# Kernel tuning notes

Hardware: AMD Instinct MI355X
Metric: run time of the kernel (lower is better)

The kernel has to match this reference:

```python
import jax, jax.numpy as jnp
import numpy as np

N_NODES = 50000
N_DIRECTED = 800000  # symmetrized to 1.6M (src,dst) pairs
IN_FEAT = 256
HEADS = 8
OUT = 64


def setup_inputs() -> dict:
    key = jax.random.key(0)
    k1, k2, k3, k4, k5 = jax.random.split(key, 5)
    r = jax.random.randint(k1, (N_DIRECTED,), 0, N_NODES)
    c = jax.random.randint(k2, (N_DIRECTED,), 0, N_NODES)
    # symmetric adjacency (values = 1), as edge list
    src = jnp.concatenate([r, c])
    dst = jnp.concatenate([c, r])
    x = jax.random.normal(k3, (N_NODES, IN_FEAT), dtype=jnp.float32)
    Ws = jax.random.normal(k4, (HEADS, OUT, IN_FEAT), dtype=jnp.float32) * 0.05
    As = jax.random.normal(k5, (HEADS, 2 * OUT, 1), dtype=jnp.float32) * 0.05
    return {"x": x, "src": src, "dst": dst, "Ws": Ws, "As": As}


def reference(x, src, dst, Ws, As):
    H, O, F = Ws.shape
    N = x.shape[0]
    # t_nodes = inputs @ Ws^T  -> [H, N, O]
    t = jnp.einsum('nf,hof->hno', x, Ws)
    a_l = As[:, :O, 0]   # [H, O]
    a_r = As[:, O:, 0]   # [H, O]
    Al = jnp.einsum('hno,ho->hn', t, a_l)  # [H, N]
    Ar = jnp.einsum('hno,ho->hn', t, a_r)  # [H, N]
    outs = []
    for k in range(H):
        # sparse E[i,j] = Al[i] + Ar[j] on adjacency pattern
        e = Al[k][src] + Ar[k][dst]  # [E]
        # NOTE: original applies tf.sparse.softmax to E directly (its lrelu
        # tensor is computed but never used), so no leaky_relu here.
        m = jax.ops.segment_max(e, src, num_segments=N)
        ex = jnp.exp(e - m[src])
        den = jax.ops.segment_sum(ex, src, num_segments=N)
        alpha = ex / den[src]
        # sparse_dense_matmul(alphas, t_nodes[k])
        h = jax.ops.segment_sum(alpha[:, None] * t[k][dst], src, num_segments=N)
        outs.append(h)
    out = jnp.stack(outs, axis=1)          # [N, H, O]
    out = out.reshape(N, H * O)            # reduction=False -> concat heads
    return jax.nn.elu(out)
```

## Files before the change

kernel.cpp:

```cpp
#include <hip/hip_runtime.h>
#include <hip/hip_bf16.h>

#define NN 50000
#define INF 256
#define NH 8
#define OUTF 64
#define NC 512
#define NTILES 782
#define EPB 8192
#define NBK 391
#define NBX 12501

typedef __attribute__((ext_vector_type(8))) short bf16x8;
typedef __attribute__((ext_vector_type(4))) float f32x4;
typedef __attribute__((ext_vector_type(2))) float v2f;
typedef __attribute__((ext_vector_type(8))) float f32x8;

__device__ __forceinline__ unsigned short f2bf(float f){
  unsigned u = __float_as_uint(f);
  u += 0x7FFFu + ((u>>16)&1u);
  return (unsigned short)(u>>16);
}

#define GLOAD_LDS16(g, s) \
  __builtin_amdgcn_global_load_lds((const __attribute__((address_space(1))) void*)(g), \
                                   (__attribute__((address_space(3))) void*)(s), 16, 0, 0)

__global__ void k_atil(const float* __restrict__ W, const float* __restrict__ As,
                       float* __restrict__ atil, int* __restrict__ cursor){
  const int h = blockIdx.x, f = threadIdx.x;
  if (h==0 && f==0){ cursor[0]=0; cursor[1]=0; }
  float s = 0.f;
  for (int o=0;o<64;o++) s += W[((long)h*64+o)*INF + f] * As[h*128 + 64 + o];
  atil[h*256 + f] = s;
}

__global__ __launch_bounds__(256) void k_front(const float* __restrict__ x,
                                               const float* __restrict__ W,
                                               unsigned short* __restrict__ Wt,
                                               const float* __restrict__ atil,
                                               unsigned short* __restrict__ xb,
                                               float* __restrict__ eAr,
                                               const int* __restrict__ src,
                                               int* __restrict__ M,
                                               int E, int NB){
  __shared__ int hh[NBK];
  const int tid = threadIdx.x;
  const int bid = blockIdx.x;
  if (bid < 8){
    const int r = tid>>2, cb = (tid&3)*64;
    char* tile = (char*)(Wt + (size_t)bid*16384);
    const float* Wr = W + ((long)bid*64 + r)*INF;
#pragma unroll
    for (int i=0;i<16;i++){
      int c = cb + i*4;
      float4 v = *(const float4*)(Wr + c);
      ushort4 b; b.x=f2bf(v.x); b.y=f2bf(v.y); b.z=f2bf(v.z); b.w=f2bf(v.w);
      int addr = r*512 + ((((c>>3) ^ (r&7)))<<4) + ((c&7)<<1);
      *(ushort4*)(tile + addr) = b;
    }
    return;
  }
  if (bid < 8+NB){
    const int b = bid-8;
    for (int i=tid;i<NBK;i+=256) hh[i]=0;
    __syncthreads();
    const int base = b*EPB;
    const int lim = min(E-base, EPB);
    for (int i=tid;i<lim;i+=256) atomicAdd(&hh[src[base+i]>>7], 1);
    __syncthreads();
    for (int i=tid;i<NBK;i+=256) M[(long)i*NB + b] = hh[i];
    return;
  }
  const int w = tid>>6, l = tid&63;
  const long n = (long)(bid-8-NB)*4 + w;
  if (n > NN) return;
  if (n == NN){
    uint2 z; z.x=0; z.y=0;
    *(uint2*)((char*)xb + (size_t)n*512 + l*8) = z;
    if (l < 8) eAr[n*NH + l] = 0.f;
    return;
  }
  float4 v = *(const float4*)(x + n*INF + l*4);
  uint2 d;
  d.x = (unsigned)f2bf(v.x) | ((unsigned)f2bf(v.y)<<16);
  d.y = (unsigned)f2bf(v.z) | ((unsigned)f2bf(v.w)<<16);
  *(uint2*)((char*)xb + (size_t)n*512 + l*8) = d;
  float p[8];
#pragma unroll
  for (int h=0;h<8;h++){
    float4 a = *(const float4*)(atil + h*256 + l*4);
    p[h] = v.x*a.x + v.y*a.y + v.z*a.z + v.w*a.w;
  }
#pragma unroll
  for (int off=1; off<64; off<<=1){
#pragma unroll
    for (int h=0;h<8;h++) p[h] += __shfl_xor(p[h], off, 64);
  }
  if (l < 8){
    float e = p[0];
#pragma unroll
    for (int h=1;h<8;h++) if (l==h) e = p[h];
    eAr[n*NH + l] = __expf(e);
  }
}

__global__ __launch_bounds__(256) void k_bscan(int* __restrict__ M,
                                               int* __restrict__ bOff,
                                               int* __restrict__ bEnd,
                                               int* __restrict__ cursor, int NB){
  __shared__ int lds[256];
  __shared__ int sb;
  const int k = blockIdx.x, tid = threadIdx.x;
  int v = (tid<NB) ? M[(long)k*NB+tid] : 0;
  const int orig = v;
  lds[tid]=v; __syncthreads();
  for (int off=1; off<256; off<<=1){
    int a = (tid>=off)? lds[tid-off] : 0;
    __syncthreads(); lds[tid]+=a; __syncthreads();
  }
  if (tid==255){
    int tot = lds[255];
    int base = atomicAdd(&cursor[0], tot);
    sb = base;
    bOff[k] = base;
    bEnd[k] = base + tot;
  }
  __syncthreads();
  if (tid<NB) M[(long)k*NB+tid] = sb + lds[tid]-orig;
}

__global__ __launch_bounds__(256) void k_bscat(const int* __restrict__ src,
                                               const int* __restrict__ dst,
                                               const int* __restrict__ M,
                                               unsigned* __restrict__ ebuf,
                                               int E, int NB){
  __shared__ int cur[NBK];
  const int tid = threadIdx.x, b = blockIdx.x;
  for (int i=tid;i<NBK;i+=256) cur[i] = M[(long)i*NB + b];
  __syncthreads();
  const int base = b*EPB;
  const int lim = min(E-base, EPB);
  for (int i=tid;i<lim;i+=256){
    int s = src[base+i], d = dst[base+i];
    int p = atomicAdd(&cur[s>>7], 1);
    ebuf[p] = ((unsigned)d<<7) | (unsigned)(s&127);
  }
}

__global__ __launch_bounds__(256) void k_bcnt_final(const unsigned* __restrict__ ebuf,
                                                    const int* __restrict__ bOff,
                                                    const int* __restrict__ bEnd,
                                                    int* __restrict__ rbeg,
                                                    int* __restrict__ rend,
                                                    int* __restrict__ col,
                                                    int* __restrict__ cursor){
  __shared__ int h[128];
  __shared__ int s[128];
  __shared__ int cur[128];
  __shared__ int pend[128];
  __shared__ int sb;
  const int k = blockIdx.x, tid = threadIdx.x;
  if (tid<128) h[tid]=0;
  __syncthreads();
  const int beg = bOff[k], end = bEnd[k];
  for (int i=beg+tid; i<end; i+=256)
    atomicAdd(&h[(int)(ebuf[i] & 127u)], 1);
  __syncthreads();
  int pc = 0;
  if (tid<128){
    pc = (h[tid]+7)&~7;
    s[tid] = pc;
  }
  __syncthreads();
  for (int off=1; off<128; off<<=1){
    int a = (tid>=off && tid<128)? s[tid-off] : 0;
    __syncthreads();
    if (tid<128) s[tid] += a;
    __syncthreads();
  }
  if (tid==0){
    sb = atomicAdd(&cursor[1], s[127]);
  }
  __syncthreads();
  if (tid<128){
    int rp = sb + s[tid] - pc;
    rbeg[(k<<7)+tid] = rp;
    rend[(k<<7)+tid] = rp + pc;
    cur[tid] = rp;
    pend[tid] = rp + pc;
  }
  __syncthreads();
  for (int i=beg+tid; i<end; i+=256){
    unsigned e = ebuf[i];
    int p = atomicAdd(&cur[e & 127u], 1);
    col[p] = (int)(e>>7);
  }
  __syncthreads();
  if (tid<128){
    for (int i=cur[tid]; i<pend[tid]; i++) col[i] = NN;
  }
}

__global__ __launch_bounds__(256) void k_aggr2(const int* __restrict__ rbeg,
                                               const int* __restrict__ rend,
                                               const int* __restrict__ col,
                                               const unsigned short* __restrict__ xb,
                                               const float* __restrict__ eAr,
                                               unsigned short* __restrict__ g,
                                               float* __restrict__ den,
                                               int tile0){
  const int tid = threadIdx.x, l = tid&63;
  const int wv = tid>>6;
  const int fh = wv&1;
  const long n = (long)tile0*64 + blockIdx.x*2 + (wv>>1);
  if (n >= NN) return;
  const int beg = __builtin_amdgcn_readfirstlane(rbeg[n]);
  const int end = __builtin_amdgcn_readfirstlane(rend[n]);
  const char* xbp = (const char*)xb + fh*256;
  v2f acc[8] = {};
  float dnl = 0.f;
  const long l4 = (long)l*4;
  const int lw = l&7;

  for (int i=beg; i<end; i+=8){
    int cc[8];
#pragma unroll
    for (int e=0;e<8;e++) cc[e] = __builtin_amdgcn_readfirstlane(col[i+e]);
    unsigned q[8];
#pragma unroll
    for (int e=0;e<8;e++) q[e] = *(const unsigned*)(xbp + (size_t)cc[e]*512 + l4);
    float wl[8];
#pragma unroll
    for (int e=0;e<8;e++) wl[e] = eAr[(size_t)cc[e]*NH + lw];
#pragma unroll
    for (int e=0;e<8;e++) dnl += wl[e];
#pragma unroll
    for (int e=0;e<8;e++){
      f32x8 wv8 = *(const f32x8*)(eAr + (size_t)cc[e]*NH);
      v2f f01;
      f01.x = __uint_as_float(q[e]<<16);
      f01.y = __uint_as_float(q[e]&0xffff0000u);
#pragma unroll
      for (int h=0;h<8;h++){
        v2f w2; w2.x = wv8[h]; w2.y = wv8[h];
        acc[h] = __builtin_elementwise_fma(w2, f01, acc[h]);
      }
    }
  }

  const int lt = (int)(n>>6) - tile0;
  const int r  = (int)(n&63);
  char* tb = (char*)g + (size_t)lt*262144 + r*512 + fh*256 + l*4;
#pragma unroll
  for (int h=0;h<8;h++){
    unsigned d = (unsigned)f2bf(acc[h].x) | ((unsigned)f2bf(acc[h].y)<<16);
    *(unsigned*)(tb + h*32768) = d;
  }
  if (fh==0 && l < 8) den[n*NH + l] = dnl;
}

__global__ __launch_bounds__(256) void k_gemm2(const unsigned short* __restrict__ g,
                                               const unsigned short* __restrict__ Wt,
                                               const float* __restrict__ den,
                                               float* __restrict__ out,
                                               int tile0){
  __shared__ unsigned short As[16384];
  __shared__ unsigned short Bs[16384];
  __shared__ float linv[64];
  const int tid = threadIdx.x, w = tid>>6, l = tid&63;
  const int brow = tile0 + blockIdx.x;
  const int h = blockIdx.y;
  {
    const char* gb = (const char*)g + (size_t)blockIdx.x*262144 + h*32768;
    char* dstA = (char*)As + w*8192;
#pragma unroll
    for (int k=0;k<8;k++){
      int r = w*16 + k*2 + (l>>5);
      const char* sA = gb + r*512 + (((l&31) ^ (r&7))<<4);
      GLOAD_LDS16(sA, dstA + k*1024);
    }
    const char* srcB = (const char*)Wt + (size_t)h*32768 + w*8192 + l*16;
    char* dstB = (char*)Bs + w*8192;
#pragma unroll
    for (int k=0;k<8;k++) GLOAD_LDS16(srcB + k*1024, dstB + k*1024);
  }
  if (tid < 64){
    long gr = (long)brow*64 + tid;
    float dv = (gr < NN) ? den[gr*NH + h] : 1.f;
    linv[tid] = dv > 0.f ? 1.f/dv : 0.f;
  }
  asm volatile("s_waitcnt vmcnt(0)");
  __syncthreads();

  const int col = w*16 + (l&15);
  f32x4 acc[4] = {};
#pragma unroll
  for (int ks=0; ks<8; ks++){
    int chunkB = (ks*4 + (l>>4)) ^ (col&7);
    bf16x8 bfrag = *(const bf16x8*)((char*)Bs + col*512 + (chunkB<<4));
#pragma unroll
    for (int mt=0; mt<4; mt++){
      int ar_ = mt*16 + (l&15);
      int chunkA = (ks*4 + (l>>4)) ^ (ar_&7);
      bf16x8 afrag = *(const bf16x8*)((char*)As + ar_*512 + (chunkA<<4));
      acc[mt] = __builtin_amdgcn_mfma_f32_16x16x32_bf16(afrag, bfrag, acc[mt], 0,0,0);
    }
  }
#pragma unroll
  for (int mt=0; mt<4; mt++){
#pragma unroll
    for (int j=0;j<4;j++){
      int r = mt*16 + (l>>4)*4 + j;
      long gr = (long)brow*64 + r;
      if (gr < NN){
        float v = acc[mt][j] * linv[r];
        out[gr*NC + h*64 + col] = v>0.f ? v : expm1f(v);
      }
    }
  }
}

extern "C" void kernel_launch(void* const* d_in, const int* in_sizes, int n_in,
                              void* d_out, int out_size, void* d_ws, size_t ws_size,
                              hipStream_t stream){
  const float* x   = (const float*)d_in[0];
  const int*   src = (const int*)d_in[1];
  const int*   dst = (const int*)d_in[2];
  const float* Ws  = (const float*)d_in[3];
  const float* Av  = (const float*)d_in[4];
  const int E = in_sizes[1];
  const int NB = (E + EPB - 1) / EPB;

  char* ws = (char*)d_ws;
  size_t off = 0;
  auto alloc = [&](size_t bytes)->void*{
    void* p = ws + off; off += (bytes + 255) & ~(size_t)255; return p;
  };
  unsigned short* xb   = (unsigned short*)alloc((size_t)50048*512);
  float* eAr           = (float*)alloc((size_t)50048*NH*4);
  float* atil          = (float*)alloc(8*256*4);
  float* den           = (float*)alloc((size_t)50048*NH*4);
  unsigned short* Wt   = (unsigned short*)alloc((size_t)8*32768);
  int*   rbeg          = (int*)alloc(50304*4);
  int*   rend          = (int*)alloc(50304*4);
  int*   M             = (int*)alloc((size_t)NBK*256*4);
  int*   bOff          = (int*)alloc(512*4);
  int*   bEnd          = (int*)alloc(512*4);
  int*   cursor        = (int*)alloc(256);
  int*   col           = (int*)alloc(((size_t)E + 8*50048 + 64)*4);

  size_t remain = (ws_size > off + 256) ? (ws_size - off - 256) : 0;
  int chunk = (int)(remain / 262144);
  if (chunk > NTILES) chunk = NTILES;
  if (chunk < 25) chunk = 25;
  unsigned short* g = (unsigned short*)alloc((size_t)chunk*262144);
  unsigned* ebuf = (unsigned*)g;

  k_atil<<<8,256,0,stream>>>(Ws, Av, atil, cursor);
  k_front<<<8+NB+NBX,256,0,stream>>>(x, Ws, Wt, atil, xb, eAr, src, M, E, NB);
  k_bscan<<<NBK,256,0,stream>>>(M, bOff, bEnd, cursor, NB);
  k_bscat<<<NB,256,0,stream>>>(src, dst, M, ebuf, E, NB);
  k_bcnt_final<<<NBK,256,0,stream>>>(ebuf, bOff, bEnd, rbeg, rend, col, cursor);

  int tile0 = 0;
  while (tile0 < NTILES){
    int tiles = NTILES - tile0 < chunk ? NTILES - tile0 : chunk;
    k_aggr2<<<tiles*32,256,0,stream>>>(rbeg, rend, col, xb, eAr, g, den, tile0);
    k_gemm2<<<dim3(tiles,8),256,0,stream>>>(g, Wt, den, (float*)d_out, tile0);
    tile0 += tiles;
  }
}
```

Baseline: 312.3 us.

## Fuse neighbor aggregation and per-head GEMM into one kernel via LDS staging

```diff
diff --git a/kernel.cpp b/kernel.cpp
--- a/kernel.cpp
+++ b/kernel.cpp
@@ -6,7 +6,7 @@
 #define NH 8
 #define OUTF 64
 #define NC 512
-#define NTILES 782
+#define NGB 3128
 #define EPB 8192
 #define NBK 391
 #define NBX 12501
@@ -21,10 +21,6 @@
   u += 0x7FFFu + ((u>>16)&1u);
   return (unsigned short)(u>>16);
 }
-
-#define GLOAD_LDS16(g, s) \
-  __builtin_amdgcn_global_load_lds((const __attribute__((address_space(1))) void*)(g), \
-                                   (__attribute__((address_space(3))) void*)(s), 16, 0, 0)
 
 __global__ void k_atil(const float* __restrict__ W, const float* __restrict__ As,
                        float* __restrict__ atil, int* __restrict__ cursor){
@@ -202,120 +198,93 @@
   }
 }
 
-__global__ __launch_bounds__(256) void k_aggr2(const int* __restrict__ rbeg,
-                                               const int* __restrict__ rend,
-                                               const int* __restrict__ col,
-                                               const unsigned short* __restrict__ xb,
-                                               const float* __restrict__ eAr,
-                                               unsigned short* __restrict__ g,
-                                               float* __restrict__ den,
-                                               int tile0){
-  const int tid = threadIdx.x, l = tid&63;
-  const int wv = tid>>6;
-  const int fh = wv&1;
-  const long n = (long)tile0*64 + blockIdx.x*2 + (wv>>1);
-  if (n >= NN) return;
-  const int beg = __builtin_amdgcn_readfirstlane(rbeg[n]);
-  const int end = __builtin_amdgcn_readfirstlane(rend[n]);
-  const char* xbp = (const char*)xb + fh*256;
-  v2f acc[8] = {};
-  float dnl = 0.f;
+__global__ __launch_bounds__(512) void k_aggr_gemm(const int* __restrict__ rbeg,
+                                                   const int* __restrict__ rend,
+                                                   const int* __restrict__ col,
+                                                   const unsigned short* __restrict__ xb,
+                                                   const float* __restrict__ eAr,
+                                                   const unsigned short* __restrict__ Wt,
+                                                   float* __restrict__ out){
+  __shared__ char gt[16*4096];
+  __shared__ float sden[16][8];
+  const int tid = threadIdx.x, l = tid&63, wid = tid>>6;
+  const long nb = (long)blockIdx.x*16;
   const long l4 = (long)l*4;
   const int lw = l&7;
 
-  for (int i=beg; i<end; i+=8){
-    int cc[8];
-#pragma unroll
-    for (int e=0;e<8;e++) cc[e] = __builtin_amdgcn_readfirstlane(col[i+e]);
-    unsigned q[8];
-#pragma unroll
-    for (int e=0;e<8;e++) q[e] = *(const unsigned*)(xbp + (size_t)cc[e]*512 + l4);
-    float wl[8];
-#pragma unroll
-    for (int e=0;e<8;e++) wl[e] = eAr[(size_t)cc[e]*NH + lw];
-#pragma unroll
-    for (int e=0;e<8;e++) dnl += wl[e];
-#pragma unroll
-    for (int e=0;e<8;e++){
-      f32x8 wv8 = *(const f32x8*)(eAr + (size_t)cc[e]*NH);
-      v2f f01;
-      f01.x = __uint_as_float(q[e]<<16);
-      f01.y = __uint_as_float(q[e]&0xffff0000u);
-#pragma unroll
-      for (int h=0;h<8;h++){
-        v2f w2; w2.x = wv8[h]; w2.y = wv8[h];
-        acc[h] = __builtin_elementwise_fma(w2, f01, acc[h]);
+  for (int t=0; t<4; t++){
+    const int task = wid*4 + t;
+    const int r  = task>>1, fh = task&1;
+    const long n = nb + r;
+    const int beg = __builtin_amdgcn_readfirstlane(rbeg[n]);
+    const int end = __builtin_amdgcn_readfirstlane(rend[n]);
+    const char* xbp = (const char*)xb + fh*256;
+    v2f acc[8] = {};
+    float dnl = 0.f;
+    for (int i=beg; i<end; i+=8){
+      int cc[8];
+#pragma unroll
+      for (int e=0;e<8;e++) cc[e] = __builtin_amdgcn_readfirstlane(col[i+e]);
+      unsigned q[8];
+#pragma unroll
+      for (int e=0;e<8;e++) q[e] = *(const unsigned*)(xbp + (size_t)cc[e]*512 + l4);
+      float wl[8];
+#pragma unroll
+      for (int e=0;e<8;e++) wl[e] = eAr[(size_t)cc[e]*NH + lw];
+#pragma unroll
+      for (int e=0;e<8;e++) dnl += wl[e];
+#pragma unroll
+      for (int e=0;e<8;e++){
+        f32x8 wv8 = *(const f32x8*)(eAr + (size_t)cc[e]*NH);
+        v2f f01;
+        f01.x = __uint_as_float(q[e]<<16);
+        f01.y = __uint_as_float(q[e]&0xffff0000u);
+#pragma unroll
+        for (int h=0;h<8;h++){
+          v2f w2; w2.x = wv8[h]; w2.y = wv8[h];
+          acc[h] = __builtin_elementwise_fma(w2, f01, acc[h]);
+        }
       }
     }
-  }
-
-  const int lt = (int)(n>>6) - tile0;
-  const int r  = (int)(n&63);
-  char* tb = (char*)g + (size_t)lt*262144 + r*512 + fh*256 + l*4;
-#pragma unroll
-  for (int h=0;h<8;h++){
-    unsigned d = (unsigned)f2bf(acc[h].x) | ((unsigned)f2bf(acc[h].y)<<16);
-    *(unsigned*)(tb + h*32768) = d;
-  }
-  if (fh==0 && l < 8) den[n*NH + l] = dnl;
-}
-
-__global__ __launch_bounds__(256) void k_gemm2(const unsigned short* __restrict__ g,
-                                               const unsigned short* __restrict__ Wt,
-                                               const float* __restrict__ den,
-                                               float* __restrict__ out,
-                                               int tile0){
-  __shared__ unsigned short As[16384];
-  __shared__ unsigned short Bs[16384];
-  __shared__ float linv[64];
-  const int tid = threadIdx.x, w = tid>>6, l = tid&63;
-  const int brow = tile0 + blockIdx.x;
-  const int h = blockIdx.y;
-  {
-    const char* gb = (const char*)g + (size_t)blockIdx.x*262144 + h*32768;
-    char* dstA = (char*)As + w*8192;
-#pragma unroll
-    for (int k=0;k<8;k++){
-      int r = w*16 + k*2 + (l>>5);
-      const char* sA = gb + r*512 + (((l&31) ^ (r&7))<<4);
-      GLOAD_LDS16(sA, dstA + k*1024);
-    }
-    const char* srcB = (const char*)Wt + (size_t)h*32768 + w*8192 + l*16;
-    char* dstB = (char*)Bs + w*8192;
-#pragma unroll
-    for (int k=0;k<8;k++) GLOAD_LDS16(srcB + k*1024, dstB + k*1024);
-  }
-  if (tid < 64){
-    long gr = (long)brow*64 + tid;
-    float dv = (gr < NN) ? den[gr*NH + h] : 1.f;
-    linv[tid] = dv > 0.f ? 1.f/dv : 0.f;
-  }
-  asm volatile("s_waitcnt vmcnt(0)");
-  __syncthreads();
-
-  const int col = w*16 + (l&15);
-  f32x4 acc[4] = {};
-#pragma unroll
+    char* seg = gt + r*4096;
+    const int boff = (fh*256 + l*4) ^ ((r&7)<<4);
+#pragma unroll
+    for (int h=0;h<8;h++){
+      unsigned d = (unsigned)f2bf(acc[h].x) | ((unsigned)f2bf(acc[h].y)<<16);
+      *(unsigned*)(seg + h*512 + boff) = d;
+    }
+    if (fh==0 && l<8) sden[r][l] = dnl;
+  }
+  __syncthreads();
+
+  const int h = wid;
+  const char* Wh = (const char*)Wt + (size_t)h*32768;
+  const int row = l&15;
+  f32x4 acc2[4] = {};
   for (int ks=0; ks<8; ks++){
-    int chunkB = (ks*4 + (l>>4)) ^ (col&7);
-    bf16x8 bfrag = *(const bf16x8*)((char*)Bs + col*512 + (chunkB<<4));
-#pragma unroll
-    for (int mt=0; mt<4; mt++){
-      int ar_ = mt*16 + (l&15);
-      int chunkA = (ks*4 + (l>>4)) ^ (ar_&7);
-      bf16x8 afrag = *(const bf16x8*)((char*)As + ar_*512 + (chunkA<<4));
-      acc[mt] = __builtin_amdgcn_mfma_f32_16x16x32_bf16(afrag, bfrag, acc[mt], 0,0,0);
-    }
-  }
-#pragma unroll
-  for (int mt=0; mt<4; mt++){
+    const int ck = ks*4 + (l>>4);
+    bf16x8 af = *(const bf16x8*)(gt + row*4096 + h*512 + ((ck ^ (row&7))<<4));
+#pragma unroll
+    for (int ct=0; ct<4; ct++){
+      const int c = ct*16 + row;
+      bf16x8 bfr = *(const bf16x8*)(Wh + c*512 + ((ck ^ (c&7))<<4));
+      acc2[ct] = __builtin_amdgcn_mfma_f32_16x16x32_bf16(af, bfr, acc2[ct], 0,0,0);
+    }
+  }
+  float lv[4];
+#pragma unroll
+  for (int j=0;j<4;j++){
+    float dv = sden[(l>>4)*4 + j][h];
+    lv[j] = dv>0.f ? 1.f/dv : 0.f;
+  }
+#pragma unroll
+  for (int ct=0; ct<4; ct++){
 #pragma unroll
     for (int j=0;j<4;j++){
-      int r = mt*16 + (l>>4)*4 + j;
-      long gr = (long)brow*64 + r;
+      long gr = nb + (l>>4)*4 + j;
       if (gr < NN){
-        float v = acc[mt][j] * linv[r];
-        out[gr*NC + h*64 + col] = v>0.f ? v : expm1f(v);
+        float v = acc2[ct][j] * lv[j];
+        out[gr*NC + h*64 + ct*16 + row] = v>0.f ? v : expm1f(v);
       }
     }
   }
@@ -340,7 +309,6 @@
   unsigned short* xb   = (unsigned short*)alloc((size_t)50048*512);
   float* eAr           = (float*)alloc((size_t)50048*NH*4);
   float* atil          = (float*)alloc(8*256*4);
-  float* den           = (float*)alloc((size_t)50048*NH*4);
   unsigned short* Wt   = (unsigned short*)alloc((size_t)8*32768);
   int*   rbeg          = (int*)alloc(50304*4);
   int*   rend          = (int*)alloc(50304*4);
@@ -349,25 +317,12 @@
   int*   bEnd          = (int*)alloc(512*4);
   int*   cursor        = (int*)alloc(256);
   int*   col           = (int*)alloc(((size_t)E + 8*50048 + 64)*4);
-
-  size_t remain = (ws_size > off + 256) ? (ws_size - off - 256) : 0;
-  int chunk = (int)(remain / 262144);
-  if (chunk > NTILES) chunk = NTILES;
-  if (chunk < 25) chunk = 25;
-  unsigned short* g = (unsigned short*)alloc((size_t)chunk*262144);
-  unsigned* ebuf = (unsigned*)g;
+  unsigned* ebuf       = (unsigned*)alloc((size_t)E*4);
 
   k_atil<<<8,256,0,stream>>>(Ws, Av, atil, cursor);
   k_front<<<8+NB+NBX,256,0,stream>>>(x, Ws, Wt, atil, xb, eAr, src, M, E, NB);
   k_bscan<<<NBK,256,0,stream>>>(M, bOff, bEnd, cursor, NB);
   k_bscat<<<NB,256,0,stream>>>(src, dst, M, ebuf, E, NB);
   k_bcnt_final<<<NBK,256,0,stream>>>(ebuf, bOff, bEnd, rbeg, rend, col, cursor);
-
-  int tile0 = 0;
-  while (tile0 < NTILES){
-    int tiles = NTILES - tile0 < chunk ? NTILES - tile0 : chunk;
-    k_aggr2<<<tiles*32,256,0,stream>>>(rbeg, rend, col, xb, eAr, g, den, tile0);
-    k_gemm2<<<dim3(tiles,8),256,0,stream>>>(g, Wt, den, (float*)d_out, tile0);
-    tile0 += tiles;
-  }
-}
+  k_aggr_gemm<<<NGB,512,0,stream>>>(rbeg, rend, col, xb, eAr, Wt, (float*)d_out);
+}
```

Result: slower. 318.6 us (+2.0%).
